# Kernel optimization log

Measured on AMD Instinct MI355X. Metric: run time of the kernel, lower is better.

The kernel has to match this reference:

```python
import jax, jax.numpy as jnp
import numpy as np


def setup_inputs() -> dict:
    key = jax.random.key(0)
    k1, k2 = jax.random.split(key)
    N, C = 8, 3
    H, W = 256, 256          # kernel-prediction grid
    KSIZE = 5                # kernels channel dim = 4 * KSIZE**2 = 100
    feat_in = jax.random.normal(k1, (N, C, 2 * H, 2 * W), dtype=jnp.float32)
    kernel = jax.random.normal(k2, (N, 4 * KSIZE * KSIZE, H, W), dtype=jnp.float32)
    return {"feat_in": feat_in, "kernel": kernel, "ksize": KSIZE}


def reference(feat_in, kernel, ksize):
    """Faithful JAX port of the customized FAC (filter-adaptive convolution).

    feat_in: (N, 3, 2H, 2W)  high-res features
    kernel : (N, 4*ksize^2, H, W)  per-pixel predicted filter taps
    output : (N, 3, H, W)
    """
    N, C, H2, W2 = feat_in.shape
    _, kch, H, W = kernel.shape
    pad = (ksize - 1) // 2

    # F.pad(..., mode='replicate')
    fp = jnp.pad(feat_in, ((0, 0), (0, 0), (pad, pad), (pad, pad)), mode='edge')

    # torch unfold(2, ksize, 1).unfold(3, ksize, 1) -> (N, C, H2, W2, kh, kw)
    patches = jnp.stack(
        [jnp.stack([fp[:, :, i:i + H2, j:j + W2] for j in range(ksize)], axis=-1)
         for i in range(ksize)], axis=-2)

    # permute(0,2,3,1,5,4) -> (N, H2, W2, C, kw, kh); contiguous reshape
    # reinterprets the (2H, 2W, C, k, k) block as (H, W, C, 4k^2)
    x = jnp.transpose(patches, (0, 2, 3, 1, 5, 4))
    x = x.reshape(N, H, W, C, ksize * ksize * 4)

    # kernel path (channels == 3, kernels == 4k^2 branch)
    k = jnp.transpose(kernel, (0, 2, 3, 1)).reshape(N, H, W, 1, 2 * ksize, 2 * ksize)
    k = jnp.concatenate([k, k, k], axis=3)              # broadcast to 3 channels
    k = jnp.transpose(k, (0, 1, 2, 3, 5, 4)).reshape(N, H, W, C, -1)

    out = jnp.sum(x * k, axis=-1)                       # (N, H, W, C)
    return jnp.transpose(out, (0, 3, 1, 2))             # (N, C, H, W)
```

## Files before the change

### kernel.cpp

```cpp
#include <hip/hip_runtime.h>


#define HH 256
#define WW 256
#define H2 512
#define W2 512
#define KPLANE (HH * WW)
#define KP4 (KPLANE / 4)

typedef float f32x4_t __attribute__((ext_vector_type(4)));

__global__ __launch_bounds__(256, 2) void fac_fused4(const float* __restrict__ feat,
                                                     const float* __restrict__ kern,
                                                     float* __restrict__ out) {
    int t  = blockIdx.x * 256 + threadIdx.x;
    int qp = t & 63;
    int h  = (t >> 6) & 255;
    int n  = t >> 14;
    int w  = qp << 2;

    int hi = (qp >> 5) & 1;
    int xb = (qp & 31) << 4;
    int y2 = 2 * h + hi;

    bool e0 = (qp & 31) == 0;
    bool e1 = (qp & 31) == 31;
    int wbase = e0 ? 0 : (e1 ? 488 : (xb - 4));

    const f32x4_t* kp4 = (const f32x4_t*)(kern + (size_t)n * 100 * KPLANE +
                                          (size_t)h * WW + w);

    const int d_tab[4][3] = {{0,1,2},{0,1,3},{0,2,3},{1,2,3}};
    const int c_tab[4][3] = {{0,1,2},{1,2,0},{2,0,1},{0,1,2}};

    float acc[3][4] = {};

#pragma unroll 1
    for (int i = 0; i < 5; ++i) {
        int sy = min(max(y2 + i - 2, 0), H2 - 1);

        float fr[3][20];
#pragma unroll
        for (int c = 0; c < 3; ++c) {
            const float* rp = feat + ((size_t)(n * 3 + c) * H2 + sy) * W2 + wbase;
            float4 q0 = *(const float4*)(rp);
            float4 q1 = *(const float4*)(rp + 4);
            float4 q2 = *(const float4*)(rp + 8);
            float4 q3 = *(const float4*)(rp + 12);
            float4 q4 = *(const float4*)(rp + 16);
            float4 q5 = *(const float4*)(rp + 20);
            float win[24] = {q0.x, q0.y, q0.z, q0.w, q1.x, q1.y, q1.z, q1.w,
                             q2.x, q2.y, q2.z, q2.w, q3.x, q3.y, q3.z, q3.w,
                             q4.x, q4.y, q4.z, q4.w, q5.x, q5.y, q5.z, q5.w};
#pragma unroll
            for (int o = 0; o < 20; ++o) {
                const int i_in = o + 2;
                const int i_e0 = (o - 2) < 0 ? 0 : (o - 2);
                const int i_e1 = (o + 6) > 23 ? 23 : (o + 6);
                fr[c][o] = e0 ? win[i_e0] : (e1 ? win[i_e1] : win[i_in]);
            }
        }

        const f32x4_t* kpi = kp4 + (size_t)i * 10 * KP4;
#pragma unroll
        for (int tb = 0; tb < 4; ++tb) {
#pragma unroll
            for (int j = 0; j < 5; ++j) {
                const int a5 = 5 * tb + j;
                const int kc = (a5 & 1) * 50 + (a5 >> 1);
                f32x4_t kv = __builtin_nontemporal_load(kpi + (size_t)kc * KP4);

                const int d0 = d_tab[tb][0], c0 = c_tab[tb][0];
                const int d1 = d_tab[tb][1], c1 = c_tab[tb][1];
                const int d2 = d_tab[tb][2], c2 = c_tab[tb][2];
#pragma unroll
                for (int p = 0; p < 4; ++p) {
                    acc[0][p] += kv[p] * fr[c0][d0 + j + 4 * p];
                    acc[1][p] += kv[p] * fr[c1][d1 + j + 4 * p];
                    acc[2][p] += kv[p] * fr[c2][d2 + j + 4 * p];
                }
            }
        }
    }

    float* op = out + (size_t)n * 3 * KPLANE + (size_t)h * WW + w;
#pragma unroll
    for (int c = 0; c < 3; ++c) {
        *(float4*)(op + (size_t)c * KPLANE) =
            make_float4(acc[c][0], acc[c][1], acc[c][2], acc[c][3]);
    }
}

extern "C" void kernel_launch(void* const* d_in, const int* in_sizes, int n_in,
                              void* d_out, int out_size, void* d_ws, size_t ws_size,
                              hipStream_t stream) {
    const float* feat = (const float*)d_in[0];
    const float* kern = (const float*)d_in[1];
    float* out = (float*)d_out;

    fac_fused4<<<512, 256, 0, stream>>>(feat, kern, out);
}
```

Baseline: 45.05 us.

## Split tap loop across two thread halves and reduce partial sums via LDS

```diff
diff --git a/kernel.cpp b/kernel.cpp
--- a/kernel.cpp
+++ b/kernel.cpp
@@ -10,13 +10,44 @@
 
 typedef float f32x4_t __attribute__((ext_vector_type(4)));
 
-__global__ __launch_bounds__(256, 2) void fac_fused4(const float* __restrict__ feat,
-                                                     const float* __restrict__ kern,
-                                                     float* __restrict__ out) {
-    int t  = blockIdx.x * 256 + threadIdx.x;
-    int qp = t & 63;
-    int h  = (t >> 6) & 255;
-    int n  = t >> 14;
+template <int TB0>
+__device__ __forceinline__ void taps2(const f32x4_t* __restrict__ kpi,
+                                      const float (&fr)[3][20], float (&acc)[3][4]) {
+    constexpr int d_tab[4][3] = {{0,1,2},{0,1,3},{0,2,3},{1,2,3}};
+    constexpr int c_tab[4][3] = {{0,1,2},{1,2,0},{2,0,1},{0,1,2}};
+#pragma unroll
+    for (int tt = 0; tt < 2; ++tt) {
+        const int tb = TB0 + tt;
+#pragma unroll
+        for (int j = 0; j < 5; ++j) {
+            const int a5 = 5 * tb + j;
+            const int kc = (a5 & 1) * 50 + (a5 >> 1);
+            f32x4_t kv = __builtin_nontemporal_load(kpi + (size_t)kc * KP4);
+            const int d0 = d_tab[tb][0], c0 = c_tab[tb][0];
+            const int d1 = d_tab[tb][1], c1 = c_tab[tb][1];
+            const int d2 = d_tab[tb][2], c2 = c_tab[tb][2];
+#pragma unroll
+            for (int p = 0; p < 4; ++p) {
+                acc[0][p] += kv[p] * fr[c0][d0 + j + 4 * p];
+                acc[1][p] += kv[p] * fr[c1][d1 + j + 4 * p];
+                acc[2][p] += kv[p] * fr[c2][d2 + j + 4 * p];
+            }
+        }
+    }
+}
+
+__global__ __launch_bounds__(512, 4) void fac_fused4s(const float* __restrict__ feat,
+                                                      const float* __restrict__ kern,
+                                                      float* __restrict__ out) {
+    __shared__ float lds[256][13];
+
+    int tid = threadIdx.x;
+    int si  = tid >> 8;
+    int lp  = tid & 255;
+    int pt  = blockIdx.x * 256 + lp;
+    int qp = pt & 63;
+    int h  = (pt >> 6) & 255;
+    int n  = pt >> 14;
     int w  = qp << 2;
 
     int hi = (qp >> 5) & 1;
@@ -29,9 +60,6 @@
 
     const f32x4_t* kp4 = (const f32x4_t*)(kern + (size_t)n * 100 * KPLANE +
                                           (size_t)h * WW + w);
-
-    const int d_tab[4][3] = {{0,1,2},{0,1,3},{0,2,3},{1,2,3}};
-    const int c_tab[4][3] = {{0,1,2},{1,2,0},{2,0,1},{0,1,2}};
 
     float acc[3][4] = {};
 
@@ -62,32 +90,28 @@
         }
 
         const f32x4_t* kpi = kp4 + (size_t)i * 10 * KP4;
-#pragma unroll
-        for (int tb = 0; tb < 4; ++tb) {
-#pragma unroll
-            for (int j = 0; j < 5; ++j) {
-                const int a5 = 5 * tb + j;
-                const int kc = (a5 & 1) * 50 + (a5 >> 1);
-                f32x4_t kv = __builtin_nontemporal_load(kpi + (size_t)kc * KP4);
-
-                const int d0 = d_tab[tb][0], c0 = c_tab[tb][0];
-                const int d1 = d_tab[tb][1], c1 = c_tab[tb][1];
-                const int d2 = d_tab[tb][2], c2 = c_tab[tb][2];
-#pragma unroll
-                for (int p = 0; p < 4; ++p) {
-                    acc[0][p] += kv[p] * fr[c0][d0 + j + 4 * p];
-                    acc[1][p] += kv[p] * fr[c1][d1 + j + 4 * p];
-                    acc[2][p] += kv[p] * fr[c2][d2 + j + 4 * p];
-                }
-            }
-        }
+        if (si == 0) taps2<0>(kpi, fr, acc);
+        else         taps2<2>(kpi, fr, acc);
     }
 
-    float* op = out + (size_t)n * 3 * KPLANE + (size_t)h * WW + w;
+    if (si == 1) {
 #pragma unroll
-    for (int c = 0; c < 3; ++c) {
-        *(float4*)(op + (size_t)c * KPLANE) =
-            make_float4(acc[c][0], acc[c][1], acc[c][2], acc[c][3]);
+        for (int c = 0; c < 3; ++c)
+#pragma unroll
+            for (int p = 0; p < 4; ++p)
+                lds[lp][c * 4 + p] = acc[c][p];
+    }
+    __syncthreads();
+    if (si == 0) {
+        float* op = out + (size_t)n * 3 * KPLANE + (size_t)h * WW + w;
+#pragma unroll
+        for (int c = 0; c < 3; ++c) {
+            *(float4*)(op + (size_t)c * KPLANE) =
+                make_float4(acc[c][0] + lds[lp][c * 4 + 0],
+                            acc[c][1] + lds[lp][c * 4 + 1],
+                            acc[c][2] + lds[lp][c * 4 + 2],
+                            acc[c][3] + lds[lp][c * 4 + 3]);
+        }
     }
 }
 
@@ -98,5 +122,5 @@
     const float* kern = (const float*)d_in[1];
     float* out = (float*)d_out;
 
-    fac_fused4<<<512, 256, 0, stream>>>(feat, kern, out);
+    fac_fused4s<<<512, 512, 0, stream>>>(feat, kern, out);
 }
```

New measurement: 84.43 us. 87.4% more time.
